# Kernel optimization log

Measured on AMD Instinct MI355X. Metric: run time of the kernel, lower is better.

## Reference

```python
import jax, jax.numpy as jnp
import numpy as np

HIDDEN = 4096
NUM_HEADS = 32
HEAD_DIM = HIDDEN // NUM_HEADS  # 128
ROPE_THETA = 10000.0
B, S = 1, 2048


def setup_inputs() -> dict:
    key = jax.random.key(0)
    k1, k2, k3, k4 = jax.random.split(key, 4)
    positions = jnp.broadcast_to(jnp.arange(S, dtype=jnp.int32), (B, S))
    hidden_states = jax.random.normal(k1, (B, S, HIDDEN), dtype=jnp.float32)
    # fused QKV projection (bias=True), output projection (bias=False)
    w_qkv = jax.random.normal(k2, (HIDDEN, 3 * HIDDEN), dtype=jnp.float32) * (HIDDEN ** -0.5)
    b_qkv = jax.random.normal(k3, (3 * HIDDEN,), dtype=jnp.float32) * 0.01
    w_o = jax.random.normal(k4, (HIDDEN, HIDDEN), dtype=jnp.float32) * (HIDDEN ** -0.5)
    return {"positions": positions, "hidden_states": hidden_states,
            "w_qkv": w_qkv, "b_qkv": b_qkv, "w_o": w_o}


def _apply_rope(x, positions):
    # x: [B, S, N, D]; NeoX-style rotate-half RoPE, rotary_dim == head_dim
    half = HEAD_DIM // 2
    inv_freq = 1.0 / (ROPE_THETA ** (jnp.arange(0, half, dtype=jnp.float32) / half))
    angles = positions.astype(jnp.float32)[..., None] * inv_freq  # [B, S, half]
    cos = jnp.cos(angles)[:, :, None, :]  # [B, S, 1, half]
    sin = jnp.sin(angles)[:, :, None, :]
    x1, x2 = x[..., :half], x[..., half:]
    return jnp.concatenate([x1 * cos - x2 * sin, x2 * cos + x1 * sin], axis=-1)


def reference(positions, hidden_states, w_qkv, b_qkv, w_o):
    qkv = jnp.einsum('bsh,hd->bsd', hidden_states, w_qkv) + b_qkv  # [B, S, 3H]
    q, k, v = jnp.split(qkv, 3, axis=-1)
    q = q.reshape(B, S, NUM_HEADS, HEAD_DIM)
    k = k.reshape(B, S, NUM_HEADS, HEAD_DIM)
    v = v.reshape(B, S, NUM_HEADS, HEAD_DIM)
    q = _apply_rope(q, positions)
    k = _apply_rope(k, positions)
    scale = HEAD_DIM ** -0.5
    scores = jnp.einsum('bqnd,bknd->bnqk', q, k) * scale  # [B, N, S, S]
    causal = jnp.tril(jnp.ones((S, S), dtype=bool))
    scores = jnp.where(causal, scores, jnp.finfo(scores.dtype).min)
    probs = jax.nn.softmax(scores, axis=-1)
    attn = jnp.einsum('bnqk,bknd->bqnd', probs, v).reshape(B, S, HIDDEN)
    return jnp.einsum('bsh,ho->bso', attn, w_o)
```

## Files before the change

### kernel.cpp

```cpp
#include <hip/hip_runtime.h>
#include <hip/hip_bf16.h>

#define S_LEN 2048
#define HID   4096
#define NH    32
#define HD    128
#define KD    4096

typedef __attribute__((ext_vector_type(4))) float f32x4;
typedef __attribute__((ext_vector_type(8))) short s16x8;
typedef __attribute__((ext_vector_type(4))) short s16x4;

#define AS1 __attribute__((address_space(1)))
#define AS3 __attribute__((address_space(3)))

__device__ __forceinline__ void gl_lds16(const void* g, void* l) {
  __builtin_amdgcn_global_load_lds((const AS1 void*)g, (AS3 void*)l, 16, 0, 0);
}

__device__ inline short f2bf(float f) {
  union { float f; unsigned u; } v; v.f = f;
  return (short)((v.u + 0x7fffu + ((v.u >> 16) & 1u)) >> 16);
}
__device__ inline float bf2f(short s) {
  union { unsigned u; float f; } v; v.u = ((unsigned)(unsigned short)s) << 16;
  return v.f;
}

__global__ __launch_bounds__(256)
void cvt_kernel(const float* __restrict__ A, short* __restrict__ Ab) {
  const size_t i = ((size_t)blockIdx.x * 256 + threadIdx.x) * 8;
  f32x4 v0 = *(const f32x4*)&A[i];
  f32x4 v1 = *(const f32x4*)&A[i + 4];
  s16x8 r;
  r[0]=f2bf(v0[0]); r[1]=f2bf(v0[1]); r[2]=f2bf(v0[2]); r[3]=f2bf(v0[3]);
  r[4]=f2bf(v1[0]); r[5]=f2bf(v1[1]); r[6]=f2bf(v1[2]); r[7]=f2bf(v1[3]);
  *(s16x8*)&Ab[i] = r;
}

__global__ __launch_bounds__(256)
void transcvt_kernel(const float* __restrict__ W, short* __restrict__ Wt, const int N) {
  __shared__ float tile[64][65];
  const int k0 = blockIdx.x * 64, n0 = blockIdx.y * 64;
  const int t = threadIdx.x;
#pragma unroll
  for (int i = 0; i < 16; ++i) {
    const int e = i * 256 + t;
    const int k = e >> 6, n = e & 63;
    tile[n][k] = W[(size_t)(k0 + k) * N + n0 + n];
  }
  __syncthreads();
  const int nn = t >> 2, ks = (t & 3) * 16;
  s16x8 a, b;
#pragma unroll
  for (int i = 0; i < 8; i++) a[i] = f2bf(tile[nn][ks + i]);
#pragma unroll
  for (int i = 0; i < 8; i++) b[i] = f2bf(tile[nn][ks + 8 + i]);
  *(s16x8*)&Wt[(size_t)(n0 + nn) * KD + k0 + ks]     = a;
  *(s16x8*)&Wt[(size_t)(n0 + nn) * KD + k0 + ks + 8] = b;
}

template<int EPI>
__global__ __launch_bounds__(256, 2)
void gemm5_kernel(const short* __restrict__ A, const short* __restrict__ Bt,
                  const float* __restrict__ bias,
                  short* __restrict__ Qb, short* __restrict__ Kb, short* __restrict__ Vb,
                  float* __restrict__ Cout)
{
  __shared__ char sm[3][24576] __attribute__((aligned(128)));
  const int KD2 = KD * 2;
  const int bid = blockIdx.x;
  const int xcd = bid & 7, idx = bid >> 3;
  const int m0 = (idx & 7) * 256;
  const int n0 = (xcd * ((EPI == 0) ? 12 : 4) + (idx >> 3)) * 128;

  const int t = threadIdx.x, lane = t & 63, c = lane & 15, g = lane >> 4;
  const int w = t >> 6, wr = w >> 1, wc = w & 1;
  const int flip = ((c >> 1) & 7) << 4;
  const int laneA = wr * 8192 + ((c * 64 + g * 16) ^ flip);
  const int laneB = 16384 + wc * 4096 + ((c * 64 + g * 16) ^ flip);

  const char* srcA[4];
  const char* srcB[2];
#pragma unroll
  for (int j = 0; j < 4; ++j) {
    const int la = j * 4096 + t * 16;
    const int ls = la ^ ((la >> 3) & 0x70);
    srcA[j] = (const char*)A + (size_t)(m0 + (ls >> 6)) * KD2 + (ls & 63);
  }
#pragma unroll
  for (int j = 0; j < 2; ++j) {
    const int la = j * 4096 + t * 16;
    const int ls = la ^ ((la >> 3) & 0x70);
    srcB[j] = (const char*)Bt + (size_t)(n0 + (ls >> 6)) * KD2 + (ls & 63);
  }

  f32x4 acc[8][4];
#pragma unroll
  for (int i = 0; i < 8; i++)
#pragma unroll
    for (int j = 0; j < 4; j++) acc[i][j] = (f32x4){0.f, 0.f, 0.f, 0.f};

#define STG(S, H) do {                                        \
    const size_t ko_ = (size_t)(H) * 64;                      \
    gl_lds16(srcA[0] + ko_, sm[S] + t * 16);                  \
    gl_lds16(srcA[1] + ko_, sm[S] + 4096  + t * 16);          \
    gl_lds16(srcA[2] + ko_, sm[S] + 8192  + t * 16);          \
    gl_lds16(srcA[3] + ko_, sm[S] + 12288 + t * 16);          \
    gl_lds16(srcB[0] + ko_, sm[S] + 16384 + t * 16);          \
    gl_lds16(srcB[1] + ko_, sm[S] + 20480 + t * 16);          \
  } while (0)

#define COMP(S) do {                                                       \
    const char* b_ = sm[S];                                                \
    s16x8 a_[8], bb_[4];                                                   \
    _Pragma("unroll")                                                      \
    for (int mi = 0; mi < 8; ++mi) a_[mi] = *(const s16x8*)(b_ + laneA + mi * 1024); \
    _Pragma("unroll")                                                      \
    for (int ni = 0; ni < 4; ++ni) bb_[ni] = *(const s16x8*)(b_ + laneB + ni * 1024); \
    __builtin_amdgcn_s_setprio(1);                                         \
    _Pragma("unroll")                                                      \
    for (int mi = 0; mi < 8; ++mi)                                         \
      _Pragma("unroll")                                                    \
      for (int ni = 0; ni < 4; ++ni)                                       \
        acc[mi][ni] = __builtin_amdgcn_mfma_f32_16x16x32_bf16(a_[mi], bb_[ni], acc[mi][ni], 0, 0, 0); \
    __builtin_amdgcn_s_setprio(0);                                         \
  } while (0)

#define WAIT6 asm volatile("s_waitcnt vmcnt(6)" ::: "memory")
#define WAIT0 asm volatile("s_waitcnt vmcnt(0)" ::: "memory")
#define BARR  do { __builtin_amdgcn_s_barrier(); asm volatile("" ::: "memory"); } while (0)

  STG(0, 0); STG(1, 1);
  for (int j = 0; j < 42; ++j) {
    const int h = 3 * j;
    WAIT6; BARR; STG(2, h + 2); COMP(0);
    WAIT6; BARR; STG(0, h + 3); COMP(1);
    WAIT6; BARR; STG(1, h + 4); COMP(2);
  }
  WAIT6; BARR; COMP(0);
  WAIT0; BARR; COMP(1);

#undef STG
#undef COMP
#undef WAIT6
#undef WAIT0
#undef BARR

  if (EPI == 0) {
#pragma unroll
    for (int ni = 0; ni < 4; ++ni) {
      const int ncol = n0 + wc * 64 + ni * 16 + c;
      const int which = ncol >> 12;
      const int h = (ncol >> 7) & 31;
      const int dcl = ncol & 127;
      short* dst = (which == 0) ? Qb : ((which == 1) ? Kb : Vb);
      const float bv = bias[ncol];
#pragma unroll
      for (int mi = 0; mi < 8; ++mi)
#pragma unroll
        for (int jj = 0; jj < 4; ++jj) {
          const int row = m0 + wr * 128 + mi * 16 + g * 4 + jj;
          dst[((size_t)h * S_LEN + row) * HD + dcl] = f2bf(acc[mi][ni][jj] + bv);
        }
    }
  } else {
#pragma unroll
    for (int ni = 0; ni < 4; ++ni) {
      const int ncol = n0 + wc * 64 + ni * 16 + c;
#pragma unroll
      for (int mi = 0; mi < 8; ++mi)
#pragma unroll
        for (int jj = 0; jj < 4; ++jj) {
          const int row = m0 + wr * 128 + mi * 16 + g * 4 + jj;
          Cout[(size_t)row * HID + ncol] = acc[mi][ni][jj];
        }
    }
  }
}

template<int EPI, int ABF16>
__global__ __launch_bounds__(256)
void gemm_kernel(const void* __restrict__ Av, const float* __restrict__ B,
                 const float* __restrict__ bias, const int N,
                 short* __restrict__ Qb, short* __restrict__ Kb, short* __restrict__ Vb,
                 float* __restrict__ Cout)
{
  __shared__ short As[128][40];
  __shared__ short Bs[128][40];
  const int m0 = blockIdx.x * 128;
  const int nb = blockIdx.y * 128;
  const int t  = threadIdx.x;
  const int w = t >> 6, lane = t & 63, c = lane & 15, g = lane >> 4;
  const int wm = (w >> 1) * 64, wn = (w & 1) * 64;

  f32x4 acc[4][4];
#pragma unroll
  for (int i = 0; i < 4; i++)
#pragma unroll
    for (int j = 0; j < 4; j++) acc[i][j] = (f32x4){0.f, 0.f, 0.f, 0.f};

  const int ar = t >> 3;
  const int ac = (t & 7) * 4;
  const int bn = t & 127;
  const int bkq = (t >> 7) * 16;

  for (int k0 = 0; k0 < KD; k0 += 32) {
#pragma unroll
    for (int rr = 0; rr < 4; rr++) {
      const int row = rr * 32 + ar;
      if (ABF16) {
        *(s16x4*)&As[row][ac] =
          *(const s16x4*)((const short*)Av + (size_t)(m0 + row) * KD + k0 + ac);
      } else {
        f32x4 v = *(const f32x4*)((const float*)Av + (size_t)(m0 + row) * KD + k0 + ac);
        s16x4 pk;
        pk[0] = f2bf(v[0]); pk[1] = f2bf(v[1]); pk[2] = f2bf(v[2]); pk[3] = f2bf(v[3]);
        *(s16x4*)&As[row][ac] = pk;
      }
    }
    const float* pB = B + (size_t)(k0 + bkq) * N + nb + bn;
    s16x8 b0, b1;
#pragma unroll
    for (int i = 0; i < 8; i++) b0[i] = f2bf(pB[(size_t)i * N]);
#pragma unroll
    for (int i = 0; i < 8; i++) b1[i] = f2bf(pB[(size_t)(i + 8) * N]);
    *(s16x8*)&Bs[bn][bkq]     = b0;
    *(s16x8*)&Bs[bn][bkq + 8] = b1;
    __syncthreads();
    s16x8 af[4], bfr[4];
#pragma unroll
    for (int i = 0; i < 4; i++) af[i]  = *(const s16x8*)&As[wm + i * 16 + c][g * 8];
#pragma unroll
    for (int i = 0; i < 4; i++) bfr[i] = *(const s16x8*)&Bs[wn + i * 16 + c][g * 8];
#pragma unroll
    for (int mi = 0; mi < 4; mi++)
#pragma unroll
      for (int ni = 0; ni < 4; ni++)
        acc[mi][ni] = __builtin_amdgcn_mfma_f32_16x16x32_bf16(af[mi], bfr[ni], acc[mi][ni], 0, 0, 0);
    __syncthreads();
  }

  if (EPI == 0) {
    const int which = nb >> 12;
    const int h = (nb & 4095) >> 7;
    short* dst = (which == 0) ? Qb : ((which == 1) ? Kb : Vb);
#pragma unroll
    for (int ni = 0; ni < 4; ni++) {
      const int d = wn + ni * 16 + c;
      const float bv = bias[nb + d];
#pragma unroll
      for (int mi = 0; mi < 4; mi++)
#pragma unroll
        for (int j = 0; j < 4; j++) {
          const int row = m0 + wm + mi * 16 + g * 4 + j;
          dst[((size_t)h * S_LEN + row) * HD + d] = f2bf(acc[mi][ni][j] + bv);
        }
    }
  } else {
#pragma unroll
    for (int ni = 0; ni < 4; ni++) {
      const int n = nb + wn + ni * 16 + c;
#pragma unroll
      for (int mi = 0; mi < 4; mi++)
#pragma unroll
        for (int j = 0; j < 4; j++) {
          const int row = m0 + wm + mi * 16 + g * 4 + j;
          Cout[(size_t)row * N + n] = acc[mi][ni][j];
        }
    }
  }
}

__global__ void rope_kernel(const int* __restrict__ positions,
                            short* __restrict__ Qb, short* __restrict__ Kb)
{
  const int s = blockIdx.x;
  const int h = blockIdx.y * 4 + threadIdx.y;
  const int d = threadIdx.x;
  const float pos = (float)positions[s];
  const float inv_freq = exp2f(-(float)d * 0.20762050593046014f);
  const float ang = pos * inv_freq;
  float sn, cs;
  sincosf(ang, &sn, &cs);
  const size_t base = ((size_t)h * S_LEN + s) * HD + d;
  const float scale = 0.08838834764831845f;
  float x1 = bf2f(Qb[base]), x2 = bf2f(Qb[base + 64]);
  Qb[base]      = f2bf((x1 * cs - x2 * sn) * scale);
  Qb[base + 64] = f2bf((x2 * cs + x1 * sn) * scale);
  x1 = bf2f(Kb[base]); x2 = bf2f(Kb[base + 64]);
  Kb[base]      = f2bf(x1 * cs - x2 * sn);
  Kb[base + 64] = f2bf(x2 * cs + x1 * sn);
}

__global__ __launch_bounds__(256)
void vtrans_kernel(const short* __restrict__ V, short* __restrict__ Vt)
{
  __shared__ short tile[64][72];
  const int h = blockIdx.z;
  const int s0 = blockIdx.x * 64;
  const int d0 = blockIdx.y * 64;
  const int tx = threadIdx.x & 63, ty = threadIdx.x >> 6;
  for (int r = ty; r < 64; r += 4)
    tile[r][tx] = V[((size_t)h * S_LEN + s0 + r) * HD + d0 + tx];
  __syncthreads();
  for (int r = ty; r < 64; r += 4)
    Vt[((size_t)h * HD + d0 + r) * S_LEN + s0 + tx] = tile[tx][r];
}

__global__ __launch_bounds__(512)
void attn_kernel(const short* __restrict__ Q, const short* __restrict__ Kg,
                 const short* __restrict__ Vtg, short* __restrict__ attn_out)
{
  __shared__ short Ks[2][32][136];
  __shared__ short Vs[2][128][40];
  __shared__ short Plds[8][16][40];
  const int h = blockIdx.y;
  const int q0 = blockIdx.x * 128;
  const int t = threadIdx.x;
  const int w = t >> 6, lane = t & 63, c = lane & 15, g = lane >> 4;
  const short* Qh = Q   + (size_t)h * S_LEN * HD;
  const short* Kh = Kg  + (size_t)h * S_LEN * HD;
  const short* Vh = Vtg + (size_t)h * HD * S_LEN;

  const int krow = t >> 4, kc16 = t & 15;
  const int vrow = t >> 2, vc16 = t & 3;

  const int qrow = q0 + w * 16 + c;
  s16x8 qf[4];
#pragma unroll
  for (int di = 0; di < 4; di++)
    qf[di] = *(const s16x8*)&Qh[(size_t)qrow * HD + di * 32 + g * 8];

  f32x4 o[8];
#pragma unroll
  for (int dt = 0; dt < 8; dt++) o[dt] = (f32x4){0.f, 0.f, 0.f, 0.f};
  float m_r[4], l_r[4];
#pragma unroll
  for (int j = 0; j < 4; j++) { m_r[j] = -3.0e38f; l_r[j] = 0.f; }

  const int nt = q0 / 32 + 4;

  {
    s16x8 gK = *(const s16x8*)&Kh[(size_t)krow * HD + kc16 * 8];
    s16x8 gV = *(const s16x8*)&Vh[(size_t)vrow * S_LEN + vc16 * 8];
    *(s16x8*)&Ks[0][krow][kc16 * 8] = gK;
    *(s16x8*)&Vs[0][vrow][vc16 * 8] = gV;
  }
  __syncthreads();

  for (int kt = 0; kt < nt; kt++) {
    const int cur = kt & 1;
    const int kb = kt * 32;
    s16x8 gK, gV;
    if (kt + 1 < nt) {
      gK = *(const s16x8*)&Kh[(size_t)(kb + 32 + krow) * HD + kc16 * 8];
      gV = *(const s16x8*)&Vh[(size_t)vrow * S_LEN + kb + 32 + vc16 * 8];
    }
    f32x4 s0 = (f32x4){0.f, 0.f, 0.f, 0.f}, s1 = (f32x4){0.f, 0.f, 0.f, 0.f};
#pragma unroll
    for (int di = 0; di < 4; di++) {
      s16x8 kf0 = *(const s16x8*)&Ks[cur][c][di * 32 + g * 8];
      s16x8 kf1 = *(const s16x8*)&Ks[cur][16 + c][di * 32 + g * 8];
      s0 = __builtin_amdgcn_mfma_f32_16x16x32_bf16(qf[di], kf0, s0, 0, 0, 0);
      s1 = __builtin_amdgcn_mfma_f32_16x16x32_bf16(qf[di], kf1, s1, 0, 0, 0);
    }
    float p0[4], p1[4], alpha[4];
#pragma unroll
    for (int j = 0; j < 4; j++) {
      const int qg = q0 + w * 16 + g * 4 + j;
      const float v0 = (kb + c      <= qg) ? s0[j] : -__builtin_inff();
      const float v1 = (kb + 16 + c <= qg) ? s1[j] : -__builtin_inff();
      float mx = fmaxf(v0, v1);
#pragma unroll
      for (int off = 1; off < 16; off <<= 1) mx = fmaxf(mx, __shfl_xor(mx, off, 64));
      const float mn = fmaxf(m_r[j], mx);
      alpha[j] = __expf(m_r[j] - mn);
      p0[j] = __expf(v0 - mn);
      p1[j] = __expf(v1 - mn);
      float rs = p0[j] + p1[j];
#pragma unroll
      for (int off = 1; off < 16; off <<= 1) rs += __shfl_xor(rs, off, 64);
      l_r[j] = l_r[j] * alpha[j] + rs;
      m_r[j] = mn;
    }
#pragma unroll
    for (int dt = 0; dt < 8; dt++)
#pragma unroll
      for (int j = 0; j < 4; j++) o[dt][j] *= alpha[j];
#pragma unroll
    for (int j = 0; j < 4; j++) {
      Plds[w][g * 4 + j][c]      = f2bf(p0[j]);
      Plds[w][g * 4 + j][16 + c] = f2bf(p1[j]);
    }
    const s16x8 pa = *(const s16x8*)&Plds[w][c][g * 8];
#pragma unroll
    for (int dt = 0; dt < 8; dt++) {
      s16x8 vf = *(const s16x8*)&Vs[cur][dt * 16 + c][g * 8];
      o[dt] = __builtin_amdgcn_mfma_f32_16x16x32_bf16(pa, vf, o[dt], 0, 0, 0);
    }
    __syncthreads();
    if (kt + 1 < nt) {
      *(s16x8*)&Ks[cur ^ 1][krow][kc16 * 8] = gK;
      *(s16x8*)&Vs[cur ^ 1][vrow][vc16 * 8] = gV;
    }
    __syncthreads();
  }

  float inv_l[4];
#pragma unroll
  for (int j = 0; j < 4; j++) inv_l[j] = 1.0f / l_r[j];
#pragma unroll
  for (int dt = 0; dt < 8; dt++)
#pragma unroll
    for (int j = 0; j < 4; j++) {
      const int row = q0 + w * 16 + g * 4 + j;
      attn_out[(size_t)row * HID + h * HD + dt * 16 + c] = f2bf(o[dt][j] * inv_l[j]);
    }
}

extern "C" void kernel_launch(void* const* d_in, const int* in_sizes, int n_in,
                              void* d_out, int out_size, void* d_ws, size_t ws_size,
                              hipStream_t stream)
{
  const int*   positions = (const int*)d_in[0];
  const float* hidden    = (const float*)d_in[1];
  const float* w_qkv     = (const float*)d_in[2];
  const float* b_qkv     = (const float*)d_in[3];
  const float* w_o       = (const float*)d_in[4];
  float* out = (float*)d_out;

  char* ws = (char*)d_ws;
  const size_t MB = (size_t)1 << 20;

  if (ws_size >= 224 * MB) {
    short* Ah    = (short*)(ws);
    short* Wqt   = (short*)(ws + 16 * MB);
    short* Wot   = (short*)(ws + 112 * MB);
    short* Qb    = (short*)(ws + 144 * MB);
    short* Kb    = (short*)(ws + 160 * MB);
    short* Vb    = (short*)(ws + 176 * MB);
    short* Vt    = (short*)(ws + 192 * MB);
    short* attnb = (short*)(ws + 208 * MB);

    cvt_kernel<<<4096, 256, 0, stream>>>(hidden, Ah);
    transcvt_kernel<<<dim3(KD / 64, 3 * HID / 64), 256, 0, stream>>>(w_qkv, Wqt, 3 * HID);
    transcvt_kernel<<<dim3(KD / 64, HID / 64), 256, 0, stream>>>(w_o, Wot, HID);
    gemm5_kernel<0><<<768, 256, 0, stream>>>(Ah, Wqt, b_qkv, Qb, Kb, Vb, nullptr);
    rope_kernel<<<dim3(S_LEN, NH / 4), dim3(64, 4), 0, stream>>>(positions, Qb, Kb);
    vtrans_kernel<<<dim3(S_LEN / 64, HD / 64, NH), 256, 0, stream>>>(Vb, Vt);
    attn_kernel<<<dim3(S_LEN / 128, NH), 512, 0, stream>>>(Qb, Kb, Vt, attnb);
    gemm5_kernel<1><<<256, 256, 0, stream>>>(attnb, Wot, nullptr,
                                             nullptr, nullptr, nullptr, out);
  } else {
    short* Qb    = (short*)(ws);
    short* Kb    = (short*)(ws + 16 * MB);
    short* Vb    = (short*)(ws + 32 * MB);
    short* Vt    = (short*)(ws + 48 * MB);
    short* attnb = (short*)(ws + 64 * MB);

    gemm_kernel<0, 0><<<dim3(16, 96), 256, 0, stream>>>(hidden, w_qkv, b_qkv, 3 * HID,
                                                        Qb, Kb, Vb, nullptr);
    rope_kernel<<<dim3(S_LEN, NH / 4), dim3(64, 4), 0, stream>>>(positions, Qb, Kb);
    vtrans_kernel<<<dim3(S_LEN / 64, HD / 64, NH), 256, 0, stream>>>(Vb, Vt);
    attn_kernel<<<dim3(S_LEN / 128, NH), 512, 0, stream>>>(Qb, Kb, Vt, attnb);
    gemm_kernel<1, 1><<<dim3(16, 32), 256, 0, stream>>>(attnb, w_o, nullptr, HID,
                                                        nullptr, nullptr, nullptr, out);
  }
}
```

Baseline: 565.0 us.

## Restructure attention to transposed S=K·Q^T with 64-key tiles and register P

The attention kernel now computes scores with K as the MFMA A-operand, so each lane holds one query row. This lets the softmax row max and sum use fewer cross-lane shuffles, and the probabilities stay in registers as the B-operand of the PV MFMA instead of passing through the Plds LDS buffer. The key tile grows from 32 to 64, K in LDS gets an XOR swizzle to avoid bank conflicts, and the rescale of the output accumulator is skipped unless the running max rises by more than 8. The output is also written as packed 4-wide stores. In exchange it uses more LDS and registers, which may lower occupancy, and the lazy rescale relies on exp values staying bounded.

```diff
diff --git a/kernel.cpp b/kernel.cpp
--- a/kernel.cpp
+++ b/kernel.cpp
@@ -25,6 +25,9 @@
 __device__ inline float bf2f(short s) {
   union { unsigned u; float f; } v; v.u = ((unsigned)(unsigned short)s) << 16;
   return v.f;
+}
+__device__ inline unsigned packbf(float a, float b) {
+  return (unsigned)(unsigned short)f2bf(a) | ((unsigned)(unsigned short)f2bf(b) << 16);
 }
 
 __global__ __launch_bounds__(256)
@@ -312,9 +315,8 @@
 void attn_kernel(const short* __restrict__ Q, const short* __restrict__ Kg,
                  const short* __restrict__ Vtg, short* __restrict__ attn_out)
 {
-  __shared__ short Ks[2][32][136];
-  __shared__ short Vs[2][128][40];
-  __shared__ short Plds[8][16][40];
+  __shared__ short Ks[2][64][128];
+  __shared__ short Vs[2][128][72];
   const int h = blockIdx.y;
   const int q0 = blockIdx.x * 128;
   const int t = threadIdx.x;
@@ -323,100 +325,125 @@
   const short* Kh = Kg  + (size_t)h * S_LEN * HD;
   const short* Vh = Vtg + (size_t)h * HD * S_LEN;
 
-  const int krow = t >> 4, kc16 = t & 15;
-  const int vrow = t >> 2, vc16 = t & 3;
-
-  const int qrow = q0 + w * 16 + c;
+  const int krow = t >> 4, kch = t & 15;
+  const int vrow = t >> 3, vch = t & 7;
+  const int ksw = (kch ^ ((krow & 3) | ((krow >> 1) & 4))) * 16;
+
+  const int rbase = (c >> 2) * 8 + (c & 3);
+  const int sb = (rbase & 3) | ((rbase >> 1) & 4);
+  int koff[4];
+#pragma unroll
+  for (int di = 0; di < 4; ++di) koff[di] = ((di * 4 + g) ^ sb) * 16;
+
+  const int qg = q0 + w * 16 + c;
   s16x8 qf[4];
 #pragma unroll
   for (int di = 0; di < 4; di++)
-    qf[di] = *(const s16x8*)&Qh[(size_t)qrow * HD + di * 32 + g * 8];
+    qf[di] = *(const s16x8*)&Qh[(size_t)qg * HD + di * 32 + g * 8];
 
   f32x4 o[8];
 #pragma unroll
   for (int dt = 0; dt < 8; dt++) o[dt] = (f32x4){0.f, 0.f, 0.f, 0.f};
-  float m_r[4], l_r[4];
-#pragma unroll
-  for (int j = 0; j < 4; j++) { m_r[j] = -3.0e38f; l_r[j] = 0.f; }
-
-  const int nt = q0 / 32 + 4;
+  float m_r = -3.0e38f, l_r = 0.f;
+
+  const int nt = q0 / 64 + 2;
 
   {
-    s16x8 gK = *(const s16x8*)&Kh[(size_t)krow * HD + kc16 * 8];
-    s16x8 gV = *(const s16x8*)&Vh[(size_t)vrow * S_LEN + vc16 * 8];
-    *(s16x8*)&Ks[0][krow][kc16 * 8] = gK;
-    *(s16x8*)&Vs[0][vrow][vc16 * 8] = gV;
+#pragma unroll
+    for (int i = 0; i < 2; ++i) {
+      s16x8 gK = *(const s16x8*)&Kh[(size_t)(i * 32 + krow) * HD + kch * 8];
+      s16x8 gV = *(const s16x8*)&Vh[(size_t)(i * 64 + vrow) * S_LEN + vch * 8];
+      *(s16x8*)((char*)&Ks[0][0][0] + (i * 32 + krow) * 256 + ksw) = gK;
+      *(s16x8*)&Vs[0][i * 64 + vrow][vch * 8] = gV;
+    }
   }
   __syncthreads();
 
   for (int kt = 0; kt < nt; kt++) {
     const int cur = kt & 1;
-    const int kb = kt * 32;
-    s16x8 gK, gV;
+    const int kb = kt * 64;
+    s16x8 gK0, gK1, gV0, gV1;
     if (kt + 1 < nt) {
-      gK = *(const s16x8*)&Kh[(size_t)(kb + 32 + krow) * HD + kc16 * 8];
-      gV = *(const s16x8*)&Vh[(size_t)vrow * S_LEN + kb + 32 + vc16 * 8];
-    }
-    f32x4 s0 = (f32x4){0.f, 0.f, 0.f, 0.f}, s1 = (f32x4){0.f, 0.f, 0.f, 0.f};
-#pragma unroll
-    for (int di = 0; di < 4; di++) {
-      s16x8 kf0 = *(const s16x8*)&Ks[cur][c][di * 32 + g * 8];
-      s16x8 kf1 = *(const s16x8*)&Ks[cur][16 + c][di * 32 + g * 8];
-      s0 = __builtin_amdgcn_mfma_f32_16x16x32_bf16(qf[di], kf0, s0, 0, 0, 0);
-      s1 = __builtin_amdgcn_mfma_f32_16x16x32_bf16(qf[di], kf1, s1, 0, 0, 0);
-    }
-    float p0[4], p1[4], alpha[4];
-#pragma unroll
-    for (int j = 0; j < 4; j++) {
-      const int qg = q0 + w * 16 + g * 4 + j;
-      const float v0 = (kb + c      <= qg) ? s0[j] : -__builtin_inff();
-      const float v1 = (kb + 16 + c <= qg) ? s1[j] : -__builtin_inff();
-      float mx = fmaxf(v0, v1);
-#pragma unroll
-      for (int off = 1; off < 16; off <<= 1) mx = fmaxf(mx, __shfl_xor(mx, off, 64));
-      const float mn = fmaxf(m_r[j], mx);
-      alpha[j] = __expf(m_r[j] - mn);
-      p0[j] = __expf(v0 - mn);
-      p1[j] = __expf(v1 - mn);
-      float rs = p0[j] + p1[j];
-#pragma unroll
-      for (int off = 1; off < 16; off <<= 1) rs += __shfl_xor(rs, off, 64);
-      l_r[j] = l_r[j] * alpha[j] + rs;
-      m_r[j] = mn;
-    }
-#pragma unroll
-    for (int dt = 0; dt < 8; dt++)
-#pragma unroll
-      for (int j = 0; j < 4; j++) o[dt][j] *= alpha[j];
-#pragma unroll
-    for (int j = 0; j < 4; j++) {
-      Plds[w][g * 4 + j][c]      = f2bf(p0[j]);
-      Plds[w][g * 4 + j][16 + c] = f2bf(p1[j]);
-    }
-    const s16x8 pa = *(const s16x8*)&Plds[w][c][g * 8];
+      gK0 = *(const s16x8*)&Kh[(size_t)(kb + 64 + krow) * HD + kch * 8];
+      gK1 = *(const s16x8*)&Kh[(size_t)(kb + 96 + krow) * HD + kch * 8];
+      gV0 = *(const s16x8*)&Vh[(size_t)vrow * S_LEN + kb + 64 + vch * 8];
+      gV1 = *(const s16x8*)&Vh[(size_t)(64 + vrow) * S_LEN + kb + 64 + vch * 8];
+    }
+    f32x4 sA = (f32x4){0,0,0,0}, sB = (f32x4){0,0,0,0};
+    f32x4 sC = (f32x4){0,0,0,0}, sD = (f32x4){0,0,0,0};
+    const char* kb_ = (const char*)&Ks[cur][0][0] + rbase * 256;
+#pragma unroll
+    for (int di = 0; di < 4; ++di) {
+      const char* p = kb_ + koff[di];
+      s16x8 kA = *(const s16x8*)(p);
+      s16x8 kB = *(const s16x8*)(p + 1024);
+      s16x8 kC = *(const s16x8*)(p + 8192);
+      s16x8 kD = *(const s16x8*)(p + 9216);
+      sA = __builtin_amdgcn_mfma_f32_16x16x32_bf16(kA, qf[di], sA, 0, 0, 0);
+      sB = __builtin_amdgcn_mfma_f32_16x16x32_bf16(kB, qf[di], sB, 0, 0, 0);
+      sC = __builtin_amdgcn_mfma_f32_16x16x32_bf16(kC, qf[di], sC, 0, 0, 0);
+      sD = __builtin_amdgcn_mfma_f32_16x16x32_bf16(kD, qf[di], sD, 0, 0, 0);
+    }
+    float v[16];
+#pragma unroll
+    for (int j = 0; j < 4; ++j) {
+      v[j]      = (kb + 8 * g + j      <= qg) ? sA[j] : -__builtin_inff();
+      v[4 + j]  = (kb + 8 * g + 4 + j  <= qg) ? sB[j] : -__builtin_inff();
+      v[8 + j]  = (kb + 32 + 8 * g + j     <= qg) ? sC[j] : -__builtin_inff();
+      v[12 + j] = (kb + 32 + 8 * g + 4 + j <= qg) ? sD[j] : -__builtin_inff();
+    }
+    float mx = v[0];
+#pragma unroll
+    for (int i = 1; i < 16; ++i) mx = fmaxf(mx, v[i]);
+    mx = fmaxf(mx, __shfl_xor(mx, 16, 64));
+    mx = fmaxf(mx, __shfl_xor(mx, 32, 64));
+    const float mn = fmaxf(m_r, mx);
+    if (!__all(mn - m_r <= 8.0f)) {
+      const float al = __expf(m_r - mn);
+      l_r *= al;
+#pragma unroll
+      for (int dt = 0; dt < 8; dt++)
+#pragma unroll
+        for (int j = 0; j < 4; j++) o[dt][j] *= al;
+      m_r = mn;
+    }
+    float p[16];
+    float rs = 0.f;
+#pragma unroll
+    for (int i = 0; i < 16; ++i) { p[i] = __expf(v[i] - m_r); rs += p[i]; }
+    rs += __shfl_xor(rs, 16, 64);
+    rs += __shfl_xor(rs, 32, 64);
+    l_r += rs;
+    union { s16x8 v8; unsigned u[4]; } pb0, pb1;
+    pb0.u[0] = packbf(p[0], p[1]);   pb0.u[1] = packbf(p[2], p[3]);
+    pb0.u[2] = packbf(p[4], p[5]);   pb0.u[3] = packbf(p[6], p[7]);
+    pb1.u[0] = packbf(p[8], p[9]);   pb1.u[1] = packbf(p[10], p[11]);
+    pb1.u[2] = packbf(p[12], p[13]); pb1.u[3] = packbf(p[14], p[15]);
 #pragma unroll
     for (int dt = 0; dt < 8; dt++) {
-      s16x8 vf = *(const s16x8*)&Vs[cur][dt * 16 + c][g * 8];
-      o[dt] = __builtin_amdgcn_mfma_f32_16x16x32_bf16(pa, vf, o[dt], 0, 0, 0);
+      s16x8 vf0 = *(const s16x8*)&Vs[cur][dt * 16 + c][g * 8];
+      s16x8 vf1 = *(const s16x8*)&Vs[cur][dt * 16 + c][32 + g * 8];
+      o[dt] = __builtin_amdgcn_mfma_f32_16x16x32_bf16(vf0, pb0.v8, o[dt], 0, 0, 0);
+      o[dt] = __builtin_amdgcn_mfma_f32_16x16x32_bf16(vf1, pb1.v8, o[dt], 0, 0, 0);
     }
     __syncthreads();
     if (kt + 1 < nt) {
-      *(s16x8*)&Ks[cur ^ 1][krow][kc16 * 8] = gK;
-      *(s16x8*)&Vs[cur ^ 1][vrow][vc16 * 8] = gV;
+      *(s16x8*)((char*)&Ks[cur ^ 1][0][0] + krow * 256 + ksw)        = gK0;
+      *(s16x8*)((char*)&Ks[cur ^ 1][0][0] + (32 + krow) * 256 + ksw) = gK1;
+      *(s16x8*)&Vs[cur ^ 1][vrow][vch * 8]      = gV0;
+      *(s16x8*)&Vs[cur ^ 1][64 + vrow][vch * 8] = gV1;
     }
     __syncthreads();
   }
 
-  float inv_l[4];
-#pragma unroll
-  for (int j = 0; j < 4; j++) inv_l[j] = 1.0f / l_r[j];
-#pragma unroll
-  for (int dt = 0; dt < 8; dt++)
-#pragma unroll
-    for (int j = 0; j < 4; j++) {
-      const int row = q0 + w * 16 + g * 4 + j;
-      attn_out[(size_t)row * HID + h * HD + dt * 16 + c] = f2bf(o[dt][j] * inv_l[j]);
-    }
+  const float inv_l = 1.0f / l_r;
+#pragma unroll
+  for (int dt = 0; dt < 8; dt++) {
+    s16x4 pk;
+#pragma unroll
+    for (int j = 0; j < 4; j++) pk[j] = f2bf(o[dt][j] * inv_l);
+    *(s16x4*)&attn_out[(size_t)qg * HID + h * HD + dt * 16 + g * 4] = pk;
+  }
 }
 
 extern "C" void kernel_launch(void* const* d_in, const int* in_sizes, int n_in,
```

Measured after the change: 485.3 us. 14.1% less time.
